# Kernel optimization log

Hardware: AMD Instinct MI355X
Metric: run time of the kernel (lower is better)

Reference implementation:

```python
import jax, jax.numpy as jnp
import numpy as np

B, Lc, Le, H, V = 128, 512, 512, 512, 128
PAD_IDX = 0  # ignore_index for cross entropy


def _lstm_cell(x, h, c, Wih, Whh, bih, bhh):
    # PyTorch gate order: i, f, g, o
    gates = x @ Wih.T + h @ Whh.T + bih + bhh
    i, f, g, o = jnp.split(gates, 4, axis=-1)
    c_new = jax.nn.sigmoid(f) * c + jax.nn.sigmoid(i) * jnp.tanh(g)
    h_new = jax.nn.sigmoid(o) * jnp.tanh(c_new)
    return h_new, c_new


def setup_inputs() -> dict:
    key = jax.random.key(0)
    ks = jax.random.split(key, 16)
    s = 0.05  # weight init scale
    inp = {
        "C": jax.random.normal(ks[0], (B, Lc, V), jnp.float32),
        "C_pad": jax.random.randint(ks[1], (B, Lc), 0, 2, jnp.int32).at[:, 0].set(0),
        "E": jax.random.randint(ks[2], (B, Le), 0, V, jnp.int32),
        "E_emb": jax.random.normal(ks[3], (B, Le, V), jnp.float32),
        # encoder LSTM (input V -> hidden H)
        "enc_Wih": s * jax.random.normal(ks[4], (4 * H, V), jnp.float32),
        "enc_Whh": s * jax.random.normal(ks[5], (4 * H, H), jnp.float32),
        "enc_bih": jnp.zeros((4 * H,), jnp.float32),
        "enc_bhh": jnp.zeros((4 * H,), jnp.float32),
        # decoder LSTMCell (input V+H -> hidden H); input is concat([E_emb_t, V_prev])
        "dec_Wih": s * jax.random.normal(ks[6], (4 * H, V + H), jnp.float32),
        "dec_Whh": s * jax.random.normal(ks[7], (4 * H, H), jnp.float32),
        "dec_bih": jnp.zeros((4 * H,), jnp.float32),
        "dec_bhh": jnp.zeros((4 * H,), jnp.float32),
        # attention_proj: Linear(H, H, bias=False)
        "att_W": s * jax.random.normal(ks[8], (H, H), jnp.float32),
        # output_proj: Linear(2H, H)
        "out_W": s * jax.random.normal(ks[9], (H, 2 * H), jnp.float32),
        "out_b": jnp.zeros((H,), jnp.float32),
        # vocab_proj: Linear(H, V)
        "voc_W": s * jax.random.normal(ks[10], (V, H), jnp.float32),
        "voc_b": jnp.zeros((V,), jnp.float32),
    }
    return inp


def reference(C, C_pad, E, E_emb, enc_Wih, enc_Whh, enc_bih, enc_bhh,
              dec_Wih, dec_Whh, dec_bih, dec_bhh, att_W, out_W, out_b,
              voc_W, voc_b):
    Bv = C.shape[0]
    Hh = enc_Whh.shape[1]

    # ---- encoder LSTM over compressed input ----
    def enc_step(carry, x_t):
        h, c = carry
        h, c = _lstm_cell(x_t, h, c, enc_Wih, enc_Whh, enc_bih, enc_bhh)
        return (h, c), h

    h0 = jnp.zeros((Bv, Hh), C.dtype)
    (hT, cT), enc_hs = jax.lax.scan(enc_step, (h0, h0), jnp.swapaxes(C, 0, 1))
    enc_hs = jnp.swapaxes(enc_hs, 0, 1)  # (B, Lc, H)
    pad = C_pad.astype(bool)              # (B, Lc)

    # ---- decoder loop (training mode, teacher forcing) ----
    def dec_step(carry, e_t):
        h, c, Vprev = carry
        x = jnp.concatenate([e_t, Vprev], axis=1)  # (B, V+H)
        h, c = _lstm_cell(x, h, c, dec_Wih, dec_Whh, dec_bih, dec_bhh)
        q = h @ att_W.T                                    # (B, H)
        scores = jnp.einsum('blh,bh->bl', enc_hs, q)       # (B, Lc)
        scores = jnp.where(pad, -jnp.inf, scores)
        d = jax.nn.softmax(scores, axis=1)
        attn = jnp.einsum('bl,blh->bh', d, enc_hs)         # (B, H)
        U = jnp.concatenate([h, attn], axis=1)             # (B, 2H)
        Vnew = U @ out_W.T + out_b                         # (B, H)
        # dropout treated as identity (eval-mode determinism)
        logits = jnp.tanh(Vnew) @ voc_W.T + voc_b          # (B, V)
        return (h, c, Vnew), logits

    Vinit = jnp.zeros((Bv, Hh), C.dtype)
    _, logits = jax.lax.scan(dec_step, (hT, cT, Vinit),
                             jnp.swapaxes(E_emb[:, :-1], 0, 1))
    logits = jnp.swapaxes(logits, 0, 1)  # (B, Le-1, V)

    # ---- cross entropy with ignore_index=PAD_IDX ----
    targets = E[:, 1:].astype(jnp.int32)
    logp = jax.nn.log_softmax(logits, axis=-1)
    nll = -jnp.take_along_axis(logp, targets[..., None], axis=-1)[..., 0]
    mask = (targets != PAD_IDX).astype(nll.dtype)
    loss = jnp.sum(nll * mask) / jnp.maximum(jnp.sum(mask), 1.0)
    return loss
```

## Files before the change

### kernel.cpp

```cpp
#include <hip/hip_runtime.h>
#include <hip/hip_bf16.h>


#define NWG 256
#define NT  256

typedef unsigned short u16;
typedef unsigned int   u32;
typedef unsigned long long u64;
typedef __attribute__((ext_vector_type(4))) float f4;
typedef __attribute__((ext_vector_type(8))) short s8;

constexpr int Bv=128, Lc=512, Le=512, Hd=512, Vc=128;
constexpr int KE=640, KD=1152;
constexpr int CAP = 144;
constexpr int SPN = 24;

constexpr size_t O_WENC = 8192;
constexpr size_t O_WDEC = O_WENC + (size_t)2048*KE*2;
constexpr size_t O_WDF  = O_WDEC + (size_t)2048*KD*2;
constexpr size_t O_ATWT = O_WDF  + (size_t)2048*KD*2;
constexpr size_t O_OUTW = O_ATWT + (size_t)512*512*2;
constexpr size_t O_VOCW = O_OUTW + (size_t)512*1024*2;
constexpr size_t O_BE   = O_VOCW + (size_t)128*512*2;
constexpr size_t O_BD   = O_BE + 8192;
constexpr size_t O_BDF  = O_BD + 8192;
constexpr size_t O_H    = O_BDF + 8192;
constexpr size_t O_TNH  = O_H + (size_t)2*128*512*2;
constexpr size_t O_PFX  = O_TNH + (size_t)2*128*512*2;
constexpr size_t O_CNT  = O_PFX + (size_t)128*512*4;
constexpr size_t O_PMS  = O_CNT + 512;
constexpr size_t O_PACC = O_PMS + 2048;
constexpr size_t O_REC  = O_PACC + (size_t)256*512*2;
constexpr size_t O_LOSS = O_REC + (size_t)2*128*2*4*4;
constexpr size_t O_ENC  = O_LOSS + 256;
constexpr size_t O_PSP  = O_ENC + (size_t)128*512*512*2;

constexpr int SC       = CAP*1024;
constexpr int SM_BYTES = SC + 16384;

struct P {
  const float *C; const int *Cpad; const int *E; const float *Eemb;
  const float *eWih,*eWhh,*ebih,*ebhh;
  const float *dWih,*dWhh,*dbih,*dbhh;
  const float *attW,*outW,*outb,*vocW,*vocb;
  char* ws; float* out;
};

__device__ inline u16 f2bf(float x){
  u32 u = __float_as_uint(x);
  return (u16)((u + 0x7fffu + ((u>>16)&1u)) >> 16);
}
__device__ inline float bf2f(u16 b){ return __uint_as_float(((u32)b)<<16); }
__device__ inline float sigm(float x){ return 1.f/(1.f+expf(-x)); }
__device__ inline f4 MM(s8 a, s8 b, f4 c){
  return __builtin_amdgcn_mfma_f32_16x16x32_bf16(a, b, c, 0, 0, 0);
}
__device__ inline u64 ld64a(const void* p){
  return __hip_atomic_load((const u64*)p, __ATOMIC_RELAXED, __HIP_MEMORY_SCOPE_AGENT);
}
__device__ inline u32 ld32u(const void* p){
  return __hip_atomic_load((const u32*)p, __ATOMIC_RELAXED, __HIP_MEMORY_SCOPE_AGENT);
}
__device__ inline void st64a(void* p, u64 v){
  __hip_atomic_store((u64*)p, v, __ATOMIC_RELAXED, __HIP_MEMORY_SCOPE_AGENT);
}
__device__ inline void st32a(void* p, u32 v){
  __hip_atomic_store((u32*)p, v, __ATOMIC_RELAXED, __HIP_MEMORY_SCOPE_AGENT);
}
__device__ inline s8 ld16a(const void* p){
  union { u64 q[2]; s8 v; } u;
  u.q[0] = ld64a(p); u.q[1] = ld64a((const char*)p + 8);
  return u.v;
}
__device__ inline s8 cvt8(const float* p){
  f4 u = *(const f4*)p, v = *(const f4*)(p+4);
  s8 r;
  r[0]=(short)f2bf(u[0]); r[1]=(short)f2bf(u[1]); r[2]=(short)f2bf(u[2]); r[3]=(short)f2bf(u[3]);
  r[4]=(short)f2bf(v[0]); r[5]=(short)f2bf(v[1]); r[6]=(short)f2bf(v[2]); r[7]=(short)f2bf(v[3]);
  return r;
}
__device__ inline float wredmax(float v){
  #pragma unroll
  for (int m=32;m;m>>=1) v = fmaxf(v, __shfl_xor(v,m,64));
  return v;
}
__device__ inline float wredsum(float v){
  #pragma unroll
  for (int m=32;m;m>>=1) v += __shfl_xor(v,m,64);
  return v;
}

extern "C" __global__ void __launch_bounds__(NT,1) k_main(P p)
{
  extern __shared__ char sm[];
  const int wg = blockIdx.x, tid = threadIdx.x;
  const int gt = wg*NT + tid;
  const int rg = wg >> 5, cg = wg & 31;

  char* ws = p.ws;
  u32*  slotA = (u32*)ws;
  u32*  slotR = (u32*)(ws + 1024 + rg*128);
  u32*  dslot = (u32*)(ws + 4096 + rg*128);
  u16*  wenc = (u16*)(ws + O_WENC);
  u16*  wdec = (u16*)(ws + O_WDEC);
  u16*  wdf  = (u16*)(ws + O_WDF);
  u16*  atwt = (u16*)(ws + O_ATWT);
  u16*  outw = (u16*)(ws + O_OUTW);
  u16*  vocw = (u16*)(ws + O_VOCW);
  float* be  = (float*)(ws + O_BE);
  float* bd  = (float*)(ws + O_BD);
  float* bdf = (float*)(ws + O_BDF);
  u16*  hbf  = (u16*)(ws + O_H);
  u16*  tnhb = (u16*)(ws + O_TNH);
  u32*  pfx  = (u32*)(ws + O_PFX);
  u32*  cntp = (u32*)(ws + O_CNT);
  u64*  pms  = (u64*)(ws + O_PMS);
  u16*  pacc16 = (u16*)(ws + O_PACC);
  float* rec = (float*)(ws + O_REC);
  float* losp= (float*)(ws + O_LOSS);
  u16*  encc = (u16*)(ws + O_ENC);
  u16*  spl  = (u16*)(ws + O_PSP) + (size_t)wg*SPN*Hd;

  u32 genA = 0, genG = 0;
  auto GBall = [&](){
    genA++;
    __syncthreads();
    if (tid == 0){
      __builtin_amdgcn_fence(__ATOMIC_RELEASE, "agent");
      st32a(slotA + wg, genA);
    }
    if (tid < 64){
      bool done = false;
      while (!done){
        u32 v0 = ld32u(slotA + tid);
        u32 v1 = ld32u(slotA + 64 + tid);
        u32 v2 = ld32u(slotA + 128 + tid);
        u32 v3 = ld32u(slotA + 192 + tid);
        done = __all((v0>=genA)&&(v1>=genA)&&(v2>=genA)&&(v3>=genA));
        if (!done) __builtin_amdgcn_s_sleep(4);
      }
      __builtin_amdgcn_fence(__ATOMIC_ACQUIRE, "agent");
    }
    __syncthreads();
  };
  auto RGB = [&](){
    genG++;
    __syncthreads();
    if (tid == 0) st32a(slotR + cg, genG);
    if (tid < 64){
      bool done = false;
      while (!done){
        u32 v = ld32u(slotR + (tid & 31));
        done = __all(v >= genG);
        if (!done) __builtin_amdgcn_s_sleep(2);
      }
      __builtin_amdgcn_fence(__ATOMIC_ACQUIRE, "workgroup");
    }
    __syncthreads();
  };

  for (int i = gt; i < 2048*KE; i += NWG*NT){
    int row = i / KE, k = i - row*KE;
    float v = (k < 128) ? p.eWih[row*128 + k] : p.eWhh[row*512 + (k-128)];
    wenc[i] = f2bf(v);
  }
  for (int i = gt; i < 2048*KD; i += NWG*NT){
    int row = i / KD, k = i - row*KD;
    float v = (k < 640) ? p.dWih[row*640 + k] : p.dWhh[row*512 + (k-640)];
    wdec[i] = f2bf(v);
  }
  for (int i = gt; i < 512*512;  i += NWG*NT){
    int kk = i >> 9, j = i & 511;
    atwt[i] = f2bf(p.attW[(size_t)j*512 + kk]);
  }
  for (int i = gt; i < 512*1024; i += NWG*NT) outw[i] = f2bf(p.outW[i]);
  for (int i = gt; i < 128*512;  i += NWG*NT) vocw[i] = f2bf(p.vocW[i]);
  for (int i = gt; i < 2048;     i += NWG*NT){ be[i] = p.ebih[i]+p.ebhh[i]; bd[i] = p.dbih[i]+p.dbhh[i]; }
  { u32* hz = (u32*)hbf; for (int i = gt; i < 65536; i += NWG*NT) hz[i] = 0; }
  if (gt == 0){ losp[0] = 0.f; losp[1] = 0.f; }

  {
    const int g0 = wg*8;
    float* dv = (float*)sm;
    for (int i = tid; i < 8*512; i += NT)
      dv[i] = p.dWih[(size_t)(g0 + (i>>9))*640 + 128 + (i&511)];
    __syncthreads();
    float wa[8][4];
    #pragma unroll
    for (int r=0;r<8;r++){ wa[r][0]=0;wa[r][1]=0;wa[r][2]=0;wa[r][3]=0; }
    for (int o = 0; o < 512; o++){
      float b0 = p.outW[(size_t)o*1024 + tid];
      float b1 = p.outW[(size_t)o*1024 + 256 + tid];
      float b2 = p.outW[(size_t)o*1024 + 512 + tid];
      float b3 = p.outW[(size_t)o*1024 + 768 + tid];
      #pragma unroll
      for (int r=0;r<8;r++){
        float d = dv[r*512+o];
        wa[r][0] += d*b0; wa[r][1] += d*b1; wa[r][2] += d*b2; wa[r][3] += d*b3;
      }
    }
    #pragma unroll
    for (int r=0;r<8;r++){
      int g = g0 + r;
      #pragma unroll
      for (int j=0;j<4;j++){
        int c = tid + 256*j;
        if (c < 512) wdf[(size_t)g*KD + 128 + c] = f2bf(p.dWhh[(size_t)g*512 + c] + wa[r][j]);
        else         wdf[(size_t)g*KD + 640 + (c-512)] = f2bf(wa[r][j]);
      }
    }
    for (int i = tid; i < 8*128; i += NT){
      int r = i >> 7, k = i & 127;
      wdf[(size_t)(g0+r)*KD + k] = f2bf(p.dWih[(size_t)(g0+r)*640 + k]);
    }
    if (tid < 8){
      int g = g0 + tid;
      float s = p.dbih[g] + p.dbhh[g];
      for (int o = 0; o < 512; o++) s += dv[tid*512+o]*p.outb[o];
      bdf[g] = s;
    }
    __syncthreads();
  }

  if (wg < 128){
    int* padl = (int*)(sm + SC);
    for (int i = tid; i < 512; i += NT) padl[i] = p.Cpad[wg*512 + i];
    __syncthreads();
    if (tid == 0){
      u32 run = 0;
      for (int tt = 0; tt < 512; tt++){ pfx[wg*512+tt] = run; if (padl[tt] == 0) run++; }
      cntp[wg] = run;
    }
    __syncthreads();
  }
  GBall();

  const int l  = tid & 63, wv = tid >> 6;
  const int n2 = wv >> 1, k2 = wv & 1;
  const int kl = (l>>4) << 3;
  const int ar = rg*16 + (l&15);
  float cst = 0.f;
  float accN = 0.f, accC = 0.f;

  const int rowA = rg*16 + (cg >> 1), halfA = cg & 1;
  const int cnA = (int)cntp[rowA], c2A = cnA >> 1;
  const int loA = halfA ? c2A : 0;
  const int mynA = (halfA ? cnA : c2A) - loA;
  const int ncapA = mynA < CAP ? mynA : CAP;
  const int limA  = mynA < CAP+SPN ? mynA : CAP+SPN;
  u16* eP = (u16*)sm;

  auto CEREC = [&](int tl){
    u32* th16 = (u32*)(sm + SC + 11776);
    float* lgp = (float*)(sm + SC + 12800);
    float* lgh = (float*)(sm + SC + 13824);
    const u16* tb = tnhb + (size_t)(tl&1)*Bv*Hd + (size_t)rowA*Hd;
    th16[tid] = ld32u(tb + 2*tid);
    __syncthreads();
    {
      int v = tid & 63, ksl = tid >> 6;
      int gv = halfA*64 + v;
      const u16* wp = vocw + (size_t)gv*Hd + ksl*128;
      const u16* hp = (const u16*)th16 + ksl*128;
      float acc = 0.f;
      #pragma unroll 4
      for (int j = 0; j < 16; j++){
        s8 wv8 = *(const s8*)(wp + j*8);
        #pragma unroll
        for (int q = 0; q < 8; q++) acc += bf2f((u16)wv8[q]) * bf2f(hp[j*8+q]);
      }
      lgp[ksl*64 + v] = acc;
    }
    __syncthreads();
    if (tid < 64){
      int gv = halfA*64 + tid;
      float lv = lgp[tid] + lgp[64+tid] + lgp[128+tid] + lgp[192+tid] + p.vocb[gv];
      lgh[tid] = lv;
      float m = wredmax(lv);
      float s = wredsum(expf(lv - m));
      if (tid == 0){
        int tgt = p.E[rowA*Le + tl + 1];
        float tlg = (tgt >= halfA*64 && tgt < halfA*64+64) ? lgh[tgt - halfA*64] : 0.f;
        float* rp = rec + ((size_t)(tl&1)*256 + rowA*2 + halfA)*4;
        union { u64 q; float f[2]; } pk; pk.f[0]=m; pk.f[1]=s;
        st64a(rp, pk.q);
        st32a(rp+2, __float_as_uint(tlg));
      }
    }
    __syncthreads();
  };
  auto COMB = [&](int tl){
    int tgt = p.E[rowA*Le + tl + 1];
    if (tgt != 0){
      const float* rp = rec + ((size_t)(tl&1)*256 + rowA*2)*4;
      union { u64 q; float f[2]; } a, b;
      a.q = ld64a(rp); b.q = ld64a(rp+4);
      float tA = __uint_as_float(ld32u(rp+2)), tB = __uint_as_float(ld32u(rp+6));
      float M = fmaxf(a.f[0], b.f[0]);
      float S = a.f[1]*expf(a.f[0]-M) + b.f[1]*expf(b.f[0]-M);
      accN += logf(S) + M - (tA + tB);
      accC += 1.f;
    }
  };

  const int gR0 = (n2*2+0)*512 + cg*16 + (l&15);
  const int gR1 = (n2*2+1)*512 + cg*16 + (l&15);

  for (int t = 0; t < Lc; t++){
    const u16* hold = hbf + (t&1)*Bv*Hd;
    u16* hnew       = hbf + ((t+1)&1)*Bv*Hd;
    s8 a[10];
    if (k2 == 0){
      #pragma unroll
      for (int ks = 4; ks < 10; ks++)
        a[ks] = ld16a(hold + (size_t)ar*Hd + (ks*32 + kl - 128));
      #pragma unroll
      for (int ks = 0; ks < 4; ks++)
        a[ks] = cvt8(p.C + ((size_t)ar*Lc + t)*Vc + ks*32 + kl);
    } else {
      #pragma unroll
      for (int ks = 0; ks < 10; ks++)
        a[ks] = ld16a(hold + (size_t)ar*Hd + (192 + ks*32 + kl));
    }
    f4 acc0 = {0,0,0,0}, acc1 = {0,0,0,0};
    #pragma unroll
    for (int ks = 0; ks < 10; ks++){
      int k = k2*320 + ks*32 + kl;
      acc0 = MM(a[ks], *(const s8*)(wenc + (size_t)gR0*KE + k), acc0);
      acc1 = MM(a[ks], *(const s8*)(wenc + (size_t)gR1*KE + k), acc1);
    }
    float* exch = (float*)(sm + SC);
    #pragma unroll
    for (int r = 0; r < 4; r++){
      int row = ((l>>4)<<2) + r;
      exch[((k2*4 + n2*2+0)*16 + row)*16 + (l&15)] = acc0[r];
      exch[((k2*4 + n2*2+1)*16 + row)*16 + (l&15)] = acc1[r];
    }
    __syncthreads();
    {
      int row = tid >> 4, u = tid & 15;
      int gb = cg*16 + u;
      float gi = exch[((0)*16+row)*16+u] + exch[((4)*16+row)*16+u] + be[0*512+gb];
      float gf = exch[((1)*16+row)*16+u] + exch[((5)*16+row)*16+u] + be[1*512+gb];
      float gg = exch[((2)*16+row)*16+u] + exch[((6)*16+row)*16+u] + be[2*512+gb];
      float go = exch[((3)*16+row)*16+u] + exch[((7)*16+row)*16+u] + be[3*512+gb];
      float fi = sigm(gi), ff = sigm(gf), fg = tanhf(gg), fo = sigm(go);
      cst = ff*cst + fi*fg;
      float hn = fo * tanhf(cst);
      int b = rg*16 + row;
      u32 hb = f2bf(hn);
      u32 nb = __shfl_xor((int)hb, 1, 64);
      if ((tid & 1) == 0){
        u32 pk = hb | (nb << 16);
        st32a(hnew + (size_t)b*Hd + gb, pk);
        if (p.Cpad[b*Lc + t] == 0){
          u32 pos = pfx[b*Lc + t];
          st32a(encc + ((size_t)b*Lc + pos)*Hd + gb, pk);
        }
      }
    }
    RGB();
  }

  GBall();

  {
    const u16* erow = encc + ((size_t)rowA*Lc + loA)*Hd;
    for (int it = 0; it*16 < limA; it++){
      s8 afr[16];
      const u16* ap = erow + (size_t)(it*16 + (l&15))*Hd;
      #pragma unroll
      for (int ks = 0; ks < 16; ks++) afr[ks] = *(const s8*)(ap + ks*32 + kl);
      for (int ot = 0; ot < 8; ot++){
        int kout0 = wv*128 + ot*16;
        f4 acc = {0,0,0,0};
        #pragma unroll
        for (int ks = 0; ks < 16; ks++)
          acc = MM(afr[ks], *(const s8*)(atwt + (size_t)(kout0 + (l&15))*Hd + ks*32 + kl), acc);
        #pragma unroll
        for (int r = 0; r < 4; r++){
          int prow = it*16 + ((l>>4)<<2) + r;
          int pcol = kout0 + (l&15);
          if (prow < limA){
            u16 pv = f2bf(acc[r]);
            if (prow < CAP) eP[(size_t)prow*Hd + pcol] = pv;
            else            spl[(size_t)(prow-CAP)*Hd + pcol] = pv;
          }
        }
      }
    }
    __syncthreads();
  }

  float* exch = (float*)(sm + SC);
  float* vex  = (float*)(sm + SC + 8192);
  float* sc2  = (float*)(sm + SC + 12288);
  s8 aH[14];

  for (int t = 0; t < Le-1; t++){
    const u16* hold = hbf + (t&1)*Bv*Hd;
    u16* hnew       = hbf + ((t+1)&1)*Bv*Hd;

    if (t == 0){
      s8 a[10];
      #pragma unroll
      for (int ks = 0; ks < 10; ks++){
        int ke = (k2==0) ? ((ks<4) ? ks*32+kl : 640 + (ks-4)*32 + kl)
                         : (832 + ks*32 + kl);
        if (ke < 128) a[ks] = cvt8(p.Eemb + ((size_t)ar*Le + 0)*Vc + ke);
        else          a[ks] = ld16a(hold + (size_t)ar*Hd + (ke-640));
      }
      f4 acc0 = {0,0,0,0}, acc1 = {0,0,0,0};
      #pragma unroll
      for (int ks = 0; ks < 10; ks++){
        int ke = (k2==0) ? ((ks<4) ? ks*32+kl : 640 + (ks-4)*32 + kl)
                         : (832 + ks*32 + kl);
        acc0 = MM(a[ks], *(const s8*)(wdec + (size_t)gR0*KD + ke), acc0);
        acc1 = MM(a[ks], *(const s8*)(wdec + (size_t)gR1*KD + ke), acc1);
      }
      #pragma unroll
      for (int r = 0; r < 4; r++){
        int row = ((l>>4)<<2) + r;
        exch[((k2*4 + n2*2+0)*16 + row)*16 + (l&15)] = acc0[r];
        exch[((k2*4 + n2*2+1)*16 + row)*16 + (l&15)] = acc1[r];
      }
      __syncthreads();
      {
        int row = tid >> 4, u = tid & 15;
        int gb = cg*16 + u;
        float gi = exch[((0)*16+row)*16+u] + exch[((4)*16+row)*16+u] + bd[0*512+gb];
        float gf = exch[((1)*16+row)*16+u] + exch[((5)*16+row)*16+u] + bd[1*512+gb];
        float gg = exch[((2)*16+row)*16+u] + exch[((6)*16+row)*16+u] + bd[2*512+gb];
        float go = exch[((3)*16+row)*16+u] + exch[((7)*16+row)*16+u] + bd[3*512+gb];
        float fi = sigm(gi), ff = sigm(gf), fg = tanhf(gg), fo = sigm(go);
        cst = ff*cst + fi*fg;
        float hn = fo * tanhf(cst);
        u32 hb = f2bf(hn);
        u32 nb = __shfl_xor((int)hb, 1, 64);
        if ((tid & 1) == 0)
          st32a(hnew + (size_t)(rg*16+row)*Hd + gb, hb | (nb << 16));
      }
    } else {
      if (tid < 16){
        union { u64 q; float f[2]; } uA, uB;
        uA.q = ld64a(pms + (rg*16+tid)*2 + 0);
        uB.q = ld64a(pms + (rg*16+tid)*2 + 1);
        float M = fmaxf(uA.f[0], uB.f[0]);
        float eA = (uA.f[0] > -1e29f) ? expf(uA.f[0]-M) : 0.f;
        float eB = (uB.f[0] > -1e29f) ? expf(uB.f[0]-M) : 0.f;
        float den = uA.f[1]*eA + uB.f[1]*eB;
        sc2[tid*2]   = eA/den;
        sc2[tid*2+1] = eB/den;
      }
      __syncthreads();
      const int colc = cg*16 + (l&15);
      if (k2 == 0){
        s8 a[18];
        #pragma unroll
        for (int ks = 4; ks < 18; ks++) a[ks] = aH[ks-4];
        #pragma unroll
        for (int ks = 0; ks < 4; ks++)
          a[ks] = cvt8(p.Eemb + ((size_t)ar*Le + t)*Vc + ks*32 + kl);
        f4 acc0 = {0,0,0,0}, acc1 = {0,0,0,0}, vac = {0,0,0,0};
        #pragma unroll
        for (int ks = 0; ks < 18; ks++){
          int k = ks*32 + kl;
          acc0 = MM(a[ks], *(const s8*)(wdf + (size_t)gR0*KD + k), acc0);
          acc1 = MM(a[ks], *(const s8*)(wdf + (size_t)gR1*KD + k), acc1);
          int ck = ks - 4;
          if (ck >= 0 && ((ck & 1) == n2))
            vac = MM(a[ks], *(const s8*)(outw + (size_t)colc*1024 + ck*32 + kl), vac);
        }
        #pragma unroll
        for (int r = 0; r < 4; r++){
          int row = ((l>>4)<<2) + r;
          exch[((n2*2+0)*16 + row)*16 + (l&15)] = acc0[r];
          exch[((n2*2+1)*16 + row)*16 + (l&15)] = acc1[r];
          vex[wv*256 + row*16 + (l&15)] = vac[r];
        }
      } else {
        const u16* pA = pacc16 + (size_t)(ar*2+0)*Hd;
        const u16* pB = pacc16 + (size_t)(ar*2+1)*Hd;
        s8 h0f = aH[0], h1f = aH[1];
        f4 acc0 = {0,0,0,0}, acc1 = {0,0,0,0};
        f4 aA0 = {0,0,0,0}, aA1 = {0,0,0,0}, aB0 = {0,0,0,0}, aB1 = {0,0,0,0};
        f4 vH = {0,0,0,0}, vA = {0,0,0,0}, vB = {0,0,0,0};
        acc0 = MM(h0f, *(const s8*)(wdf + (size_t)gR0*KD + 576 + kl), acc0);
        acc1 = MM(h0f, *(const s8*)(wdf + (size_t)gR1*KD + 576 + kl), acc1);
        acc0 = MM(h1f, *(const s8*)(wdf + (size_t)gR0*KD + 608 + kl), acc0);
        acc1 = MM(h1f, *(const s8*)(wdf + (size_t)gR1*KD + 608 + kl), acc1);
        {
          s8 hf = (n2 == 0) ? h0f : h1f;
          vH = MM(hf, *(const s8*)(outw + (size_t)colc*1024 + (14+n2)*32 + kl), vH);
        }
        #pragma unroll
        for (int hb = 0; hb < 2; hb++){
          s8 pf[8];
          #pragma unroll
          for (int j = 0; j < 8; j++)
            pf[j] = ld16a(pA + (hb*8+j)*32 + kl);
          #pragma unroll
          for (int j = 0; j < 8; j++){
            int c = hb*8 + j;
            int k = 640 + c*32 + kl;
            aA0 = MM(pf[j], *(const s8*)(wdf + (size_t)gR0*KD + k), aA0);
            aA1 = MM(pf[j], *(const s8*)(wdf + (size_t)gR1*KD + k), aA1);
            if (((16 + c) & 1) == n2)
              vA = MM(pf[j], *(const s8*)(outw + (size_t)colc*1024 + (16+c)*32 + kl), vA);
          }
        }
        #pragma unroll
        for (int hb = 0; hb < 2; hb++){
          s8 pf[8];
          #pragma unroll
          for (int j = 0; j < 8; j++)
            pf[j] = ld16a(pB + (hb*8+j)*32 + kl);
          #pragma unroll
          for (int j = 0; j < 8; j++){
            int c = hb*8 + j;
            int k = 640 + c*32 + kl;
            aB0 = MM(pf[j], *(const s8*)(wdf + (size_t)gR0*KD + k), aB0);
            aB1 = MM(pf[j], *(const s8*)(wdf + (size_t)gR1*KD + k), aB1);
            if (((16 + c) & 1) == n2)
              vB = MM(pf[j], *(const s8*)(outw + (size_t)colc*1024 + (16+c)*32 + kl), vB);
          }
        }
        #pragma unroll
        for (int r = 0; r < 4; r++){
          int row = ((l>>4)<<2) + r;
          float sAr = sc2[row*2], sBr = sc2[row*2+1];
          exch[((4 + n2*2+0)*16 + row)*16 + (l&15)] = acc0[r] + sAr*aA0[r] + sBr*aB0[r];
          exch[((4 + n2*2+1)*16 + row)*16 + (l&15)] = acc1[r] + sAr*aA1[r] + sBr*aB1[r];
          vex[wv*256 + row*16 + (l&15)] = vH[r] + sAr*vA[r] + sBr*vB[r];
        }
      }
      __syncthreads();
      {
        int row = tid >> 4, u = tid & 15;
        int gb = cg*16 + u;
        float gi = exch[((0)*16+row)*16+u] + exch[((4)*16+row)*16+u] + bdf[0*512+gb];
        float gf = exch[((1)*16+row)*16+u] + exch[((5)*16+row)*16+u] + bdf[1*512+gb];
        float gg = exch[((2)*16+row)*16+u] + exch[((6)*16+row)*16+u] + bdf[2*512+gb];
        float go = exch[((3)*16+row)*16+u] + exch[((7)*16+row)*16+u] + bdf[3*512+gb];
        float fi = sigm(gi), ff = sigm(gf), fg = tanhf(gg), fo = sigm(go);
        cst = ff*cst + fi*fg;
        float hn = fo * tanhf(cst);
        u32 hb = f2bf(hn);
        u32 nb = __shfl_xor((int)hb, 1, 64);
        if ((tid & 1) == 0)
          st32a(hnew + (size_t)(rg*16+row)*Hd + gb, hb | (nb << 16));
        float v = vex[row*16+u] + vex[256+row*16+u] + vex[512+row*16+u]
                + vex[768+row*16+u] + p.outb[gb];
        u32 tb2 = f2bf(tanhf(v));
        u32 tn2 = __shfl_xor((int)tb2, 1, 64);
        if ((tid & 1) == 0){
          u16* tnw = tnhb + (size_t)((t-1)&1)*Bv*Hd;
          st32a(tnw + (size_t)(rg*16+row)*Hd + gb, tb2 | (tn2 << 16));
        }
      }
    }
    RGB();

    {
      const int ne = limA, ncap = ncapA;
      float* hld = (float*)(sm + SC);
      float* scl = (float*)(sm + SC + 2048);
      float* red = (float*)(sm + SC + 2816);
      float* part= (float*)(sm + SC + 3584);
      {
        u32 hw = ld32u(hnew + (size_t)rowA*Hd + 2*tid);
        int c0 = 2*tid, c1 = c0+1;
        hld[(c0&15)*32 + (c0>>4)] = bf2f((u16)(hw & 0xffffu));
        hld[(c1&15)*32 + (c1>>4)] = bf2f((u16)(hw >> 16));
      }
      __syncthreads();
      const int pg8 = tid >> 5, ln = tid & 31;
      int i = pg8;
      for (; i < ncap; i += 8){
        const u16* e = eP + (size_t)i*Hd + ln*16;
        s8 ev0 = *(const s8*)(e);
        s8 ev1 = *(const s8*)(e+8);
        float s = 0.f;
        #pragma unroll
        for (int j=0;j<8;j++) s += bf2f((u16)ev0[j]) * hld[j*32+ln];
        #pragma unroll
        for (int j=0;j<8;j++) s += bf2f((u16)ev1[j]) * hld[(j+8)*32+ln];
        #pragma unroll
        for (int m=1;m<32;m<<=1) s += __shfl_xor(s, m, 64);
        if (ln == 0) scl[i] = s;
      }
      for (; i < ne; i += 8){
        const u16* e = spl + (size_t)(i-CAP)*Hd + ln*16;
        s8 ev0 = *(const s8*)(e);
        s8 ev1 = *(const s8*)(e+8);
        float s = 0.f;
        #pragma unroll
        for (int j=0;j<8;j++) s += bf2f((u16)ev0[j]) * hld[j*32+ln];
        #pragma unroll
        for (int j=0;j<8;j++) s += bf2f((u16)ev1[j]) * hld[(j+8)*32+ln];
        #pragma unroll
        for (int m=1;m<32;m<<=1) s += __shfl_xor(s, m, 64);
        if (ln == 0) scl[i] = s;
      }
      __syncthreads();
      float mloc = -1e30f;
      for (int i2 = tid; i2 < ne; i2 += NT) mloc = fmaxf(mloc, scl[i2]);
      mloc = wredmax(mloc);
      if ((tid&63)==0) red[tid>>6] = mloc;
      __syncthreads();
      float M = fmaxf(fmaxf(red[0],red[1]), fmaxf(red[2],red[3]));
      __syncthreads();
      float sloc = 0.f;
      for (int i2 = tid; i2 < ne; i2 += NT){ float w = expf(scl[i2]-M); scl[i2]=w; sloc += w; }
      sloc = wredsum(sloc);
      if ((tid&63)==0) red[tid>>6] = sloc;
      __syncthreads();
      float S = red[0]+red[1]+red[2]+red[3];
      float a8[8] = {0,0,0,0,0,0,0,0};
      const u16* eb2 = encc + ((size_t)rowA*Lc + loA)*Hd + l*8;
      int ii = wv;
      for (; ii + 12 < ne; ii += 16){
        s8 e0 = *(const s8*)(eb2 + (size_t)(ii   )*Hd);
        s8 e1 = *(const s8*)(eb2 + (size_t)(ii+ 4)*Hd);
        s8 e2 = *(const s8*)(eb2 + (size_t)(ii+ 8)*Hd);
        s8 e3 = *(const s8*)(eb2 + (size_t)(ii+12)*Hd);
        float w0=scl[ii], w1=scl[ii+4], w2=scl[ii+8], w3=scl[ii+12];
        #pragma unroll
        for (int j=0;j<8;j++) a8[j] += w0*bf2f((u16)e0[j]);
        #pragma unroll
        for (int j=0;j<8;j++) a8[j] += w1*bf2f((u16)e1[j]);
        #pragma unroll
        for (int j=0;j<8;j++) a8[j] += w2*bf2f((u16)e2[j]);
        #pragma unroll
        for (int j=0;j<8;j++) a8[j] += w3*bf2f((u16)e3[j]);
      }
      for (; ii < ne; ii += 4){
        s8 e0 = *(const s8*)(eb2 + (size_t)ii*Hd);
        float w0 = scl[ii];
        #pragma unroll
        for (int j=0;j<8;j++) a8[j] += w0*bf2f((u16)e0[j]);
      }
      { f4 v0 = {a8[0],a8[1],a8[2],a8[3]}, v1 = {a8[4],a8[5],a8[6],a8[7]};
        *(f4*)(part + wv*512 + l*8)     = v0;
        *(f4*)(part + wv*512 + l*8 + 4) = v1; }
      __syncthreads();
      {
        int h0 = 2*tid;
        float a0 = part[h0] + part[512+h0] + part[1024+h0] + part[1536+h0];
        float a1 = part[h0+1] + part[512+h0+1] + part[1024+h0+1] + part[1536+h0+1];
        st32a(pacc16 + (size_t)(rowA*2+halfA)*Hd + h0, (u32)f2bf(a0) | ((u32)f2bf(a1) << 16));
        if (tid == 0){
          union { u64 q; float f[2]; } pk; pk.f[0]=M; pk.f[1]=S;
          st64a(pms + rowA*2 + halfA, pk.q);
        }
      }
      __syncthreads();
      if (t >= 1) CEREC(t-1);
      if (t >= 2 && halfA == 0 && tid == 0) COMB(t-2);
      if (t < Le-2){
        if (k2 == 0){
          #pragma unroll
          for (int ks = 4; ks < 18; ks++)
            aH[ks-4] = ld16a(hnew + (size_t)ar*Hd + (ks*32 + kl - 128));
        } else {
          aH[0] = ld16a(hnew + (size_t)ar*Hd + (448 + kl));
          aH[1] = ld16a(hnew + (size_t)ar*Hd + (480 + kl));
        }
      }
    }
    RGB();
  }

  const int TL = Le-2;
  {
    if (tid < 16){
      union { u64 q; float f[2]; } uA, uB;
      uA.q = ld64a(pms + (rg*16+tid)*2 + 0);
      uB.q = ld64a(pms + (rg*16+tid)*2 + 1);
      float M = fmaxf(uA.f[0], uB.f[0]);
      float eA = (uA.f[0] > -1e29f) ? expf(uA.f[0]-M) : 0.f;
      float eB = (uB.f[0] > -1e29f) ? expf(uB.f[0]-M) : 0.f;
      float den = uA.f[1]*eA + uB.f[1]*eB;
      sc2[tid*2]   = eA/den;
      sc2[tid*2+1] = eB/den;
    }
    __syncthreads();
    const float scA = sc2[(l&15)*2], scB = sc2[(l&15)*2+1];
    const u16* h5 = hbf + (size_t)((TL+1)&1)*Bv*Hd;
    const u16* pA = pacc16 + (size_t)(ar*2+0)*Hd;
    const u16* pB = pacc16 + (size_t)(ar*2+1)*Hd;
    const int colc = cg*16 + (l&15);
    f4 vac = {0,0,0,0};
    #pragma unroll
    for (int j = 0; j < 8; j++){
      int kv = k2*16 + j*2 + n2;
      s8 af;
      if (kv < 16) af = ld16a(h5 + (size_t)ar*Hd + kv*32 + kl);
      else {
        s8 va = ld16a(pA + (kv-16)*32 + kl);
        s8 vb = ld16a(pB + (kv-16)*32 + kl);
        #pragma unroll
        for (int q = 0; q < 8; q++)
          af[q] = (short)f2bf(scA*bf2f((u16)va[q]) + scB*bf2f((u16)vb[q]));
      }
      vac = MM(af, *(const s8*)(outw + (size_t)colc*1024 + kv*32 + kl), vac);
    }
    #pragma unroll
    for (int r = 0; r < 4; r++)
      vex[wv*256 + (((l>>4)<<2)+r)*16 + (l&15)] = vac[r];
    __syncthreads();
    {
      int row = tid >> 4, u = tid & 15;
      int gb = cg*16 + u;
      float v = vex[row*16+u] + vex[256+row*16+u] + vex[512+row*16+u]
              + vex[768+row*16+u] + p.outb[gb];
      u32 tb2 = f2bf(tanhf(v));
      u32 tn2 = __shfl_xor((int)tb2, 1, 64);
      if ((tid & 1) == 0){
        u16* tnw = tnhb + (size_t)(TL&1)*Bv*Hd;
        st32a(tnw + (size_t)(rg*16+row)*Hd + gb, tb2 | (tn2 << 16));
      }
    }
  }
  RGB();
  {
    CEREC(TL);
    if (halfA == 0 && tid == 0) COMB(TL-1);
  }
  RGB();
  {
    if (halfA == 0 && tid == 0){
      COMB(TL);
      atomicAdd(losp + 0, accN);
      atomicAdd(losp + 1, accC);
    }
  }
  GBall();
  if (wg == 0 && tid == 0) p.out[0] = losp[0] / fmaxf(losp[1], 1.f);

  for (int d = 1; d <= 2048; d++){
    __syncthreads();
    if (tid == 0) st32a(dslot + cg, (u32)d);
    if (tid < 64){
      bool done = false;
      while (!done){
        u32 v = ld32u(dslot + (tid & 31));
        done = __all(v >= (u32)d);
        if (!done) __builtin_amdgcn_s_sleep(2);
      }
    }
    __syncthreads();
  }
}

extern "C" void kernel_launch(void* const* d_in, const int* in_sizes, int n_in,
                              void* d_out, int out_size, void* d_ws, size_t ws_size,
                              hipStream_t stream)
{
  hipFuncSetAttribute(reinterpret_cast<const void*>(k_main),
                      hipFuncAttributeMaxDynamicSharedMemorySize, SM_BYTES);
  hipMemsetAsync(d_ws, 0, 8192, stream);

  P prm;
  prm.C    = (const float*)d_in[0];
  prm.Cpad = (const int*)  d_in[1];
  prm.E    = (const int*)  d_in[2];
  prm.Eemb = (const float*)d_in[3];
  prm.eWih = (const float*)d_in[4];
  prm.eWhh = (const float*)d_in[5];
  prm.ebih = (const float*)d_in[6];
  prm.ebhh = (const float*)d_in[7];
  prm.dWih = (const float*)d_in[8];
  prm.dWhh = (const float*)d_in[9];
  prm.dbih = (const float*)d_in[10];
  prm.dbhh = (const float*)d_in[11];
  prm.attW = (const float*)d_in[12];
  prm.outW = (const float*)d_in[13];
  prm.outb = (const float*)d_in[14];
  prm.vocW = (const float*)d_in[15];
  prm.vocb = (const float*)d_in[16];
  prm.ws   = (char*)d_ws;
  prm.out  = (float*)d_out;

  k_main<<<dim3(NWG), dim3(NT), SM_BYTES, stream>>>(prm);
}
```

Baseline: 23.91 ms.

## Split persistent kernel into encoder/decoder launches and drop trailing barrier loop

Splits the single persistent kernel into two launches: an encoder kernel that writes the final LSTM cell state to a new global buffer, and a decoder kernel that reads it back. The kernel boundary replaces the grid-wide barrier between the phases, and the decoder gets its own barrier slot region. It also removes a 2048-iteration cross-workgroup barrier loop that ran after the loss was written. Separately, the attention-weighted sum over encoder states is unrolled from 4 to 8 rows per iteration, with the products summed into one expression. The cost is an extra launch, a global round trip for the cell state, and more register pressure in the attention loop.

```diff
diff --git a/kernel.cpp b/kernel.cpp
--- a/kernel.cpp
+++ b/kernel.cpp
@@ -35,6 +35,7 @@
 constexpr size_t O_LOSS = O_REC + (size_t)2*128*2*4*4;
 constexpr size_t O_ENC  = O_LOSS + 256;
 constexpr size_t O_PSP  = O_ENC + (size_t)128*512*512*2;
+constexpr size_t O_CST  = O_PSP + (size_t)256*SPN*512*2;
 
 constexpr int SC       = CAP*1024;
 constexpr int SM_BYTES = SC + 16384;
@@ -91,7 +92,7 @@
   return v;
 }
 
-extern "C" __global__ void __launch_bounds__(NT,1) k_main(P p)
+extern "C" __global__ void __launch_bounds__(NT,1) k_enc(P p)
 {
   extern __shared__ char sm[];
   const int wg = blockIdx.x, tid = threadIdx.x;
@@ -101,7 +102,6 @@
   char* ws = p.ws;
   u32*  slotA = (u32*)ws;
   u32*  slotR = (u32*)(ws + 1024 + rg*128);
-  u32*  dslot = (u32*)(ws + 4096 + rg*128);
   u16*  wenc = (u16*)(ws + O_WENC);
   u16*  wdec = (u16*)(ws + O_WDEC);
   u16*  wdf  = (u16*)(ws + O_WDF);
@@ -112,15 +112,11 @@
   float* bd  = (float*)(ws + O_BD);
   float* bdf = (float*)(ws + O_BDF);
   u16*  hbf  = (u16*)(ws + O_H);
-  u16*  tnhb = (u16*)(ws + O_TNH);
   u32*  pfx  = (u32*)(ws + O_PFX);
   u32*  cntp = (u32*)(ws + O_CNT);
-  u64*  pms  = (u64*)(ws + O_PMS);
-  u16*  pacc16 = (u16*)(ws + O_PACC);
-  float* rec = (float*)(ws + O_REC);
   float* losp= (float*)(ws + O_LOSS);
   u16*  encc = (u16*)(ws + O_ENC);
-  u16*  spl  = (u16*)(ws + O_PSP) + (size_t)wg*SPN*Hd;
+  float* cstg= (float*)(ws + O_CST);
 
   u32 genA = 0, genG = 0;
   auto GBall = [&](){
@@ -241,68 +237,6 @@
   const int kl = (l>>4) << 3;
   const int ar = rg*16 + (l&15);
   float cst = 0.f;
-  float accN = 0.f, accC = 0.f;
-
-  const int rowA = rg*16 + (cg >> 1), halfA = cg & 1;
-  const int cnA = (int)cntp[rowA], c2A = cnA >> 1;
-  const int loA = halfA ? c2A : 0;
-  const int mynA = (halfA ? cnA : c2A) - loA;
-  const int ncapA = mynA < CAP ? mynA : CAP;
-  const int limA  = mynA < CAP+SPN ? mynA : CAP+SPN;
-  u16* eP = (u16*)sm;
-
-  auto CEREC = [&](int tl){
-    u32* th16 = (u32*)(sm + SC + 11776);
-    float* lgp = (float*)(sm + SC + 12800);
-    float* lgh = (float*)(sm + SC + 13824);
-    const u16* tb = tnhb + (size_t)(tl&1)*Bv*Hd + (size_t)rowA*Hd;
-    th16[tid] = ld32u(tb + 2*tid);
-    __syncthreads();
-    {
-      int v = tid & 63, ksl = tid >> 6;
-      int gv = halfA*64 + v;
-      const u16* wp = vocw + (size_t)gv*Hd + ksl*128;
-      const u16* hp = (const u16*)th16 + ksl*128;
-      float acc = 0.f;
-      #pragma unroll 4
-      for (int j = 0; j < 16; j++){
-        s8 wv8 = *(const s8*)(wp + j*8);
-        #pragma unroll
-        for (int q = 0; q < 8; q++) acc += bf2f((u16)wv8[q]) * bf2f(hp[j*8+q]);
-      }
-      lgp[ksl*64 + v] = acc;
-    }
-    __syncthreads();
-    if (tid < 64){
-      int gv = halfA*64 + tid;
-      float lv = lgp[tid] + lgp[64+tid] + lgp[128+tid] + lgp[192+tid] + p.vocb[gv];
-      lgh[tid] = lv;
-      float m = wredmax(lv);
-      float s = wredsum(expf(lv - m));
-      if (tid == 0){
-        int tgt = p.E[rowA*Le + tl + 1];
-        float tlg = (tgt >= halfA*64 && tgt < halfA*64+64) ? lgh[tgt - halfA*64] : 0.f;
-        float* rp = rec + ((size_t)(tl&1)*256 + rowA*2 + halfA)*4;
-        union { u64 q; float f[2]; } pk; pk.f[0]=m; pk.f[1]=s;
-        st64a(rp, pk.q);
-        st32a(rp+2, __float_as_uint(tlg));
-      }
-    }
-    __syncthreads();
-  };
-  auto COMB = [&](int tl){
-    int tgt = p.E[rowA*Le + tl + 1];
-    if (tgt != 0){
-      const float* rp = rec + ((size_t)(tl&1)*256 + rowA*2)*4;
-      union { u64 q; float f[2]; } a, b;
-      a.q = ld64a(rp); b.q = ld64a(rp+4);
-      float tA = __uint_as_float(ld32u(rp+2)), tB = __uint_as_float(ld32u(rp+6));
-      float M = fmaxf(a.f[0], b.f[0]);
-      float S = a.f[1]*expf(a.f[0]-M) + b.f[1]*expf(b.f[0]-M);
-      accN += logf(S) + M - (tA + tB);
-      accC += 1.f;
-    }
-  };
 
   const int gR0 = (n2*2+0)*512 + cg*16 + (l&15);
   const int gR1 = (n2*2+1)*512 + cg*16 + (l&15);
@@ -363,7 +297,152 @@
     RGB();
   }
 
-  GBall();
+  {
+    int row = tid >> 4, u = tid & 15;
+    cstg[(size_t)(rg*16+row)*Hd + cg*16 + u] = cst;
+  }
+}
+
+extern "C" __global__ void __launch_bounds__(NT,1) k_dec(P p)
+{
+  extern __shared__ char sm[];
+  const int wg = blockIdx.x, tid = threadIdx.x;
+  const int rg = wg >> 5, cg = wg & 31;
+
+  char* ws = p.ws;
+  u32*  slotA = (u32*)(ws + 2048);
+  u32*  slotR = (u32*)(ws + 4096 + rg*128);
+  u16*  wdec = (u16*)(ws + O_WDEC);
+  u16*  wdf  = (u16*)(ws + O_WDF);
+  u16*  atwt = (u16*)(ws + O_ATWT);
+  u16*  outw = (u16*)(ws + O_OUTW);
+  u16*  vocw = (u16*)(ws + O_VOCW);
+  float* bd  = (float*)(ws + O_BD);
+  float* bdf = (float*)(ws + O_BDF);
+  u16*  hbf  = (u16*)(ws + O_H);
+  u16*  tnhb = (u16*)(ws + O_TNH);
+  u32*  cntp = (u32*)(ws + O_CNT);
+  u64*  pms  = (u64*)(ws + O_PMS);
+  u16*  pacc16 = (u16*)(ws + O_PACC);
+  float* rec = (float*)(ws + O_REC);
+  float* losp= (float*)(ws + O_LOSS);
+  u16*  encc = (u16*)(ws + O_ENC);
+  u16*  spl  = (u16*)(ws + O_PSP) + (size_t)wg*SPN*Hd;
+  float* cstg= (float*)(ws + O_CST);
+
+  u32 genA = 0, genG = 0;
+  auto GBall = [&](){
+    genA++;
+    __syncthreads();
+    if (tid == 0){
+      __builtin_amdgcn_fence(__ATOMIC_RELEASE, "agent");
+      st32a(slotA + wg, genA);
+    }
+    if (tid < 64){
+      bool done = false;
+      while (!done){
+        u32 v0 = ld32u(slotA + tid);
+        u32 v1 = ld32u(slotA + 64 + tid);
+        u32 v2 = ld32u(slotA + 128 + tid);
+        u32 v3 = ld32u(slotA + 192 + tid);
+        done = __all((v0>=genA)&&(v1>=genA)&&(v2>=genA)&&(v3>=genA));
+        if (!done) __builtin_amdgcn_s_sleep(4);
+      }
+      __builtin_amdgcn_fence(__ATOMIC_ACQUIRE, "agent");
+    }
+    __syncthreads();
+  };
+  auto RGB = [&](){
+    genG++;
+    __syncthreads();
+    if (tid == 0) st32a(slotR + cg, genG);
+    if (tid < 64){
+      bool done = false;
+      while (!done){
+        u32 v = ld32u(slotR + (tid & 31));
+        done = __all(v >= genG);
+        if (!done) __builtin_amdgcn_s_sleep(2);
+      }
+      __builtin_amdgcn_fence(__ATOMIC_ACQUIRE, "workgroup");
+    }
+    __syncthreads();
+  };
+
+  const int l  = tid & 63, wv = tid >> 6;
+  const int n2 = wv >> 1, k2 = wv & 1;
+  const int kl = (l>>4) << 3;
+  const int ar = rg*16 + (l&15);
+  float accN = 0.f, accC = 0.f;
+
+  float cst;
+  {
+    int row = tid >> 4, u = tid & 15;
+    cst = cstg[(size_t)(rg*16+row)*Hd + cg*16 + u];
+  }
+
+  const int rowA = rg*16 + (cg >> 1), halfA = cg & 1;
+  const int cnA = (int)cntp[rowA], c2A = cnA >> 1;
+  const int loA = halfA ? c2A : 0;
+  const int mynA = (halfA ? cnA : c2A) - loA;
+  const int ncapA = mynA < CAP ? mynA : CAP;
+  const int limA  = mynA < CAP+SPN ? mynA : CAP+SPN;
+  u16* eP = (u16*)sm;
+
+  auto CEREC = [&](int tl){
+    u32* th16 = (u32*)(sm + SC + 11776);
+    float* lgp = (float*)(sm + SC + 12800);
+    float* lgh = (float*)(sm + SC + 13824);
+    const u16* tb = tnhb + (size_t)(tl&1)*Bv*Hd + (size_t)rowA*Hd;
+    th16[tid] = ld32u(tb + 2*tid);
+    __syncthreads();
+    {
+      int v = tid & 63, ksl = tid >> 6;
+      int gv = halfA*64 + v;
+      const u16* wp = vocw + (size_t)gv*Hd + ksl*128;
+      const u16* hp = (const u16*)th16 + ksl*128;
+      float acc = 0.f;
+      #pragma unroll 4
+      for (int j = 0; j < 16; j++){
+        s8 wv8 = *(const s8*)(wp + j*8);
+        #pragma unroll
+        for (int q = 0; q < 8; q++) acc += bf2f((u16)wv8[q]) * bf2f(hp[j*8+q]);
+      }
+      lgp[ksl*64 + v] = acc;
+    }
+    __syncthreads();
+    if (tid < 64){
+      int gv = halfA*64 + tid;
+      float lv = lgp[tid] + lgp[64+tid] + lgp[128+tid] + lgp[192+tid] + p.vocb[gv];
+      lgh[tid] = lv;
+      float m = wredmax(lv);
+      float s = wredsum(expf(lv - m));
+      if (tid == 0){
+        int tgt = p.E[rowA*Le + tl + 1];
+        float tlg = (tgt >= halfA*64 && tgt < halfA*64+64) ? lgh[tgt - halfA*64] : 0.f;
+        float* rp = rec + ((size_t)(tl&1)*256 + rowA*2 + halfA)*4;
+        union { u64 q; float f[2]; } pk; pk.f[0]=m; pk.f[1]=s;
+        st64a(rp, pk.q);
+        st32a(rp+2, __float_as_uint(tlg));
+      }
+    }
+    __syncthreads();
+  };
+  auto COMB = [&](int tl){
+    int tgt = p.E[rowA*Le + tl + 1];
+    if (tgt != 0){
+      const float* rp = rec + ((size_t)(tl&1)*256 + rowA*2)*4;
+      union { u64 q; float f[2]; } a, b;
+      a.q = ld64a(rp); b.q = ld64a(rp+4);
+      float tA = __uint_as_float(ld32u(rp+2)), tB = __uint_as_float(ld32u(rp+6));
+      float M = fmaxf(a.f[0], b.f[0]);
+      float S = a.f[1]*expf(a.f[0]-M) + b.f[1]*expf(b.f[0]-M);
+      accN += logf(S) + M - (tA + tB);
+      accC += 1.f;
+    }
+  };
+
+  const int gR0 = (n2*2+0)*512 + cg*16 + (l&15);
+  const int gR1 = (n2*2+1)*512 + cg*16 + (l&15);
 
   {
     const u16* erow = encc + ((size_t)rowA*Lc + loA)*Hd;
@@ -620,20 +699,22 @@
       float a8[8] = {0,0,0,0,0,0,0,0};
       const u16* eb2 = encc + ((size_t)rowA*Lc + loA)*Hd + l*8;
       int ii = wv;
-      for (; ii + 12 < ne; ii += 16){
-        s8 e0 = *(const s8*)(eb2 + (size_t)(ii   )*Hd);
+      for (; ii + 28 < ne; ii += 32){
+        s8 e0 = *(const s8*)(eb2 + (size_t)(ii    )*Hd);
         s8 e1 = *(const s8*)(eb2 + (size_t)(ii+ 4)*Hd);
         s8 e2 = *(const s8*)(eb2 + (size_t)(ii+ 8)*Hd);
         s8 e3 = *(const s8*)(eb2 + (size_t)(ii+12)*Hd);
+        s8 e4 = *(const s8*)(eb2 + (size_t)(ii+16)*Hd);
+        s8 e5 = *(const s8*)(eb2 + (size_t)(ii+20)*Hd);
+        s8 e6 = *(const s8*)(eb2 + (size_t)(ii+24)*Hd);
+        s8 e7 = *(const s8*)(eb2 + (size_t)(ii+28)*Hd);
         float w0=scl[ii], w1=scl[ii+4], w2=scl[ii+8], w3=scl[ii+12];
-        #pragma unroll
-        for (int j=0;j<8;j++) a8[j] += w0*bf2f((u16)e0[j]);
-        #pragma unroll
-        for (int j=0;j<8;j++) a8[j] += w1*bf2f((u16)e1[j]);
-        #pragma unroll
-        for (int j=0;j<8;j++) a8[j] += w2*bf2f((u16)e2[j]);
-        #pragma unroll
-        for (int j=0;j<8;j++) a8[j] += w3*bf2f((u16)e3[j]);
+        float w4=scl[ii+16], w5=scl[ii+20], w6=scl[ii+24], w7=scl[ii+28];
+        #pragma unroll
+        for (int j=0;j<8;j++) a8[j] += w0*bf2f((u16)e0[j]) + w1*bf2f((u16)e1[j])
+                                    + w2*bf2f((u16)e2[j]) + w3*bf2f((u16)e3[j])
+                                    + w4*bf2f((u16)e4[j]) + w5*bf2f((u16)e5[j])
+                                    + w6*bf2f((u16)e6[j]) + w7*bf2f((u16)e7[j]);
       }
       for (; ii < ne; ii += 4){
         s8 e0 = *(const s8*)(eb2 + (size_t)ii*Hd);
@@ -738,27 +819,15 @@
   }
   GBall();
   if (wg == 0 && tid == 0) p.out[0] = losp[0] / fmaxf(losp[1], 1.f);
-
-  for (int d = 1; d <= 2048; d++){
-    __syncthreads();
-    if (tid == 0) st32a(dslot + cg, (u32)d);
-    if (tid < 64){
-      bool done = false;
-      while (!done){
-        u32 v = ld32u(dslot + (tid & 31));
-        done = __all(v >= (u32)d);
-        if (!done) __builtin_amdgcn_s_sleep(2);
-      }
-    }
-    __syncthreads();
-  }
 }
 
 extern "C" void kernel_launch(void* const* d_in, const int* in_sizes, int n_in,
                               void* d_out, int out_size, void* d_ws, size_t ws_size,
                               hipStream_t stream)
 {
-  hipFuncSetAttribute(reinterpret_cast<const void*>(k_main),
+  hipFuncSetAttribute(reinterpret_cast<const void*>(k_enc),
+                      hipFuncAttributeMaxDynamicSharedMemorySize, SM_BYTES);
+  hipFuncSetAttribute(reinterpret_cast<const void*>(k_dec),
                       hipFuncAttributeMaxDynamicSharedMemorySize, SM_BYTES);
   hipMemsetAsync(d_ws, 0, 8192, stream);
 
@@ -783,5 +852,6 @@
   prm.ws   = (char*)d_ws;
   prm.out  = (float*)d_out;
 
-  k_main<<<dim3(NWG), dim3(NT), SM_BYTES, stream>>>(prm);
-}
+  k_enc<<<dim3(NWG), dim3(NT), SM_BYTES, stream>>>(prm);
+  k_dec<<<dim3(NWG), dim3(NT), SM_BYTES, stream>>>(prm);
+}
```

Result: faster. 21.57 ms (-9.8%).
